# Kernel tuning notes

Measured on AMD Instinct MI355X. Metric: run time of the kernel, lower is better.

Reference implementation:

```python
import jax, jax.numpy as jnp
import numpy as np

MAX_REL = 1024
N_HEADS = 16
HEAD_DIM = 64


def setup_inputs() -> dict:
    key = jax.random.key(0)
    ks = jax.random.split(key, 12)
    b, s, dm = 4, 1024, 1024
    sc = 1.0 / np.sqrt(dm)
    return {
        "hidden_states": jax.random.normal(ks[0], (b, s, dm), jnp.float32),
        "attention_mask": jnp.zeros((b, s), jnp.float32),
        "Wq": jax.random.normal(ks[1], (dm, dm), jnp.float32) * sc,
        "bq": jnp.zeros((dm,), jnp.float32),
        "Wk": jax.random.normal(ks[2], (dm, dm), jnp.float32) * sc,
        "bk": jnp.zeros((dm,), jnp.float32),
        "Wv": jax.random.normal(ks[3], (dm, dm), jnp.float32) * sc,
        "bv": jnp.zeros((dm,), jnp.float32),
        "Wo": jax.random.normal(ks[4], (dm, dm), jnp.float32) * sc,
        "bo": jnp.zeros((dm,), jnp.float32),
        "rel_emb": jax.random.normal(ks[5], (2 * MAX_REL + 1, HEAD_DIM), jnp.float32) * 0.02,
        "M": jax.random.uniform(ks[6], (1, N_HEADS, HEAD_DIM, HEAD_DIM), jnp.float32),
        "z": jax.random.uniform(ks[7], (1, N_HEADS, HEAD_DIM), jnp.float32),
        "gate_alpha": jax.random.uniform(ks[8], (1,), jnp.float32),
    }


def reference(hidden_states, attention_mask, Wq, bq, Wk, bk, Wv, bv, Wo, bo,
              rel_emb, M, z, gate_alpha):
    b, s, dm = hidden_states.shape
    H, D = N_HEADS, HEAD_DIM

    def proj(W, bias):
        return (hidden_states @ W + bias).reshape(b, s, H, D).transpose(0, 2, 1, 3)  # bhsd

    q = proj(Wq, bq)
    k = proj(Wk, bk)
    v = proj(Wv, bv)

    # relative-position embeddings: rel[q_pos, k_pos, d]
    ridx = jnp.clip(jnp.arange(s)[:, None] - jnp.arange(s)[None, :], -MAX_REL, MAX_REL) + MAX_REL
    rel = rel_emb[ridx]  # [s, s, D]

    # scores[b,h,q,k] = sum_d (q + rel) * k   (content + position terms, no 5-D materialization)
    scores = (jnp.einsum('bhqd,bhkd->bhqk', q, k)
              + jnp.einsum('qkd,bhkd->bhqk', rel, k)) / np.sqrt(D).astype(np.float32)
    scores = scores + attention_mask[:, None, None, :] * (-1e9)
    w = jax.nn.softmax(scores, axis=-1)
    local = jnp.einsum('bhqk,bhkd->bhqd', w, v)

    # linear-attention read of global memory (M, z)
    sq = jax.nn.elu(q) + 1.0  # [b,h,s,d]
    num = jnp.einsum('bhld,hde->bhle', sq, M[0])
    den = jnp.einsum('bhld,hd->bhl', sq, z[0]) + 1e-6
    glob = num / den[..., None]

    gate = jax.nn.sigmoid(gate_alpha[0])
    combined = gate * local + (1.0 - gate) * glob  # [b,h,s,d]
    out = combined.transpose(0, 2, 1, 3).reshape(b, s, dm) @ Wo + bo
    return out
```

## Files before the change

### kernel.cpp

```cpp
#include <hip/hip_runtime.h>
#include <cstdint>
#include <cstddef>

typedef __bf16 bf16x8 __attribute__((ext_vector_type(8)));
typedef float f32x4 __attribute__((ext_vector_type(4)));

static __device__ __forceinline__ f32x4 mfma16(bf16x8 a, bf16x8 b, f32x4 c) {
  return __builtin_amdgcn_mfma_f32_16x16x32_bf16(a, b, c, 0, 0, 0);
}


__global__ __launch_bounds__(256) void detect_k(const uint32_t* __restrict__ hs,
                                                int* __restrict__ flag) {
  __shared__ int cnt;
  if (threadIdx.x == 0) cnt = 0;
  __syncthreads();
  uint32_t w = hs[threadIdx.x];
  int b = (w >> 8) & 0x7F;
  if (b >= 0x3C && b <= 0x40) atomicAdd(&cnt, 1);
  __syncthreads();
  if (threadIdx.x == 0) *flag = (cnt >= 128) ? 1 : 0;
}

__global__ __launch_bounds__(256) void cvt_to_bf16_k(const void* __restrict__ src,
                                                     __bf16* __restrict__ dst, int n,
                                                     const int* __restrict__ flag) {
  int i = blockIdx.x * 256 + threadIdx.x;
  if (i >= n) return;
  float v = (*flag) ? (float)((const __bf16*)src)[i] : ((const float*)src)[i];
  dst[i] = (__bf16)v;
}

__global__ __launch_bounds__(256) void cvt_to_f32_k(const void* __restrict__ src,
                                                    float* __restrict__ dst, int n,
                                                    const int* __restrict__ flag) {
  int i = blockIdx.x * 256 + threadIdx.x;
  if (i >= n) return;
  dst[i] = (*flag) ? (float)((const __bf16*)src)[i] : ((const float*)src)[i];
}

__global__ void cvt_wT_k(const void* __restrict__ W, __bf16* __restrict__ T,
                         const int* __restrict__ flag) {
  __shared__ __bf16 t[32][33];
  int k0 = blockIdx.x * 32, n0 = blockIdx.y * 32;
  int tx = threadIdx.x, ty = threadIdx.y;
  int f = *flag;
#pragma unroll
  for (int i = 0; i < 32; i += 8) {
    size_t idx = (size_t)(k0 + ty + i) * 1024 + n0 + tx;
    float v = f ? (float)((const __bf16*)W)[idx] : ((const float*)W)[idx];
    t[ty + i][tx] = (__bf16)v;
  }
  __syncthreads();
#pragma unroll
  for (int i = 0; i < 32; i += 8)
    T[(size_t)(n0 + ty + i) * 1024 + k0 + tx] = t[tx][ty + i];
}

__global__ __launch_bounds__(256) void gemm_bt_k(const __bf16* __restrict__ A,
                                                 const __bf16* __restrict__ Bt,
                                                 const float* __restrict__ bias,
                                                 __bf16* __restrict__ C,
                                                 int M, int N, int K, int ldc) {
  const int tm = blockIdx.x * 128, tn = blockIdx.y * 128;
  const int tid = threadIdx.x;
  const int w = tid >> 6, l = tid & 63;
  const int l15 = l & 15, l4 = l >> 4;
  const int wm = (w >> 1) * 64, wn = (w & 1) * 64;
  __shared__ __bf16 As[128 * 64];
  __shared__ __bf16 Bs[128 * 64];
  f32x4 acc[4][4] = {};
  for (int kt = 0; kt < K; kt += 64) {
    __syncthreads();
#pragma unroll
    for (int i = 0; i < 4; ++i) {
      int c = tid + i * 256;
      int r = c >> 3, s = c & 7;
      int byt = r * 128 + ((s ^ (r & 7)) << 4);
      *(bf16x8*)((char*)As + byt) = *(const bf16x8*)(A + (size_t)(tm + r) * K + kt + s * 8);
      *(bf16x8*)((char*)Bs + byt) = *(const bf16x8*)(Bt + (size_t)(tn + r) * K + kt + s * 8);
    }
    __syncthreads();
#pragma unroll
    for (int kk = 0; kk < 2; ++kk) {
      bf16x8 af[4], bfr[4];
#pragma unroll
      for (int m = 0; m < 4; ++m) {
        int row = wm + m * 16 + l15;
        af[m] = *(const bf16x8*)((char*)As + row * 128 + (((l4 + 4 * kk) ^ (row & 7)) << 4));
      }
#pragma unroll
      for (int n = 0; n < 4; ++n) {
        int row = wn + n * 16 + l15;
        bfr[n] = *(const bf16x8*)((char*)Bs + row * 128 + (((l4 + 4 * kk) ^ (row & 7)) << 4));
      }
#pragma unroll
      for (int m = 0; m < 4; ++m)
#pragma unroll
        for (int n = 0; n < 4; ++n)
          acc[m][n] = mfma16(af[m], bfr[n], acc[m][n]);
    }
  }
#pragma unroll
  for (int m = 0; m < 4; ++m)
#pragma unroll
    for (int n = 0; n < 4; ++n) {
      int row = tm + wm + m * 16 + l4 * 4;
      int col = tn + wn + n * 16 + l15;
      float bb = bias[col];
#pragma unroll
      for (int r = 0; r < 4; ++r)
        C[(size_t)(row + r) * ldc + col] = (__bf16)(acc[m][n][r] + bb);
    }
}

__global__ __launch_bounds__(256) void gemm_bt_out_k(const __bf16* __restrict__ A,
                                                     const __bf16* __restrict__ Bt,
                                                     const float* __restrict__ bias,
                                                     void* __restrict__ out,
                                                     int M, int N, int K, int pairOff,
                                                     const int* __restrict__ flag) {
  const int tm = blockIdx.x * 128, tn = blockIdx.y * 128;
  const int tid = threadIdx.x;
  const int w = tid >> 6, l = tid & 63;
  const int l15 = l & 15, l4 = l >> 4;
  const int wm = (w >> 1) * 64, wn = (w & 1) * 64;
  __shared__ __bf16 As[128 * 64];
  __shared__ __bf16 Bs[128 * 64];
  f32x4 acc[4][4] = {};
  for (int kt = 0; kt < K; kt += 64) {
    __syncthreads();
#pragma unroll
    for (int i = 0; i < 4; ++i) {
      int c = tid + i * 256;
      int r = c >> 3, s = c & 7;
      int byt = r * 128 + ((s ^ (r & 7)) << 4);
      *(bf16x8*)((char*)As + byt) = *(const bf16x8*)(A + (size_t)(tm + r) * K + kt + s * 8);
      *(bf16x8*)((char*)Bs + byt) = *(const bf16x8*)(Bt + (size_t)(tn + r) * K + kt + s * 8);
    }
    __syncthreads();
#pragma unroll
    for (int kk = 0; kk < 2; ++kk) {
      bf16x8 af[4], bfr[4];
#pragma unroll
      for (int m = 0; m < 4; ++m) {
        int row = wm + m * 16 + l15;
        af[m] = *(const bf16x8*)((char*)As + row * 128 + (((l4 + 4 * kk) ^ (row & 7)) << 4));
      }
#pragma unroll
      for (int n = 0; n < 4; ++n) {
        int row = wn + n * 16 + l15;
        bfr[n] = *(const bf16x8*)((char*)Bs + row * 128 + (((l4 + 4 * kk) ^ (row & 7)) << 4));
      }
#pragma unroll
      for (int m = 0; m < 4; ++m)
#pragma unroll
        for (int n = 0; n < 4; ++n)
          acc[m][n] = mfma16(af[m], bfr[n], acc[m][n]);
    }
  }
  int use16 = *flag;
#pragma unroll
  for (int m = 0; m < 4; ++m)
#pragma unroll
    for (int n = 0; n < 4; ++n) {
      int row = tm + wm + m * 16 + l4 * 4;
      int col = tn + wn + n * 16 + l15;
      float bb = bias[col];
#pragma unroll
      for (int r = 0; r < 4; ++r) {
        float v = acc[m][n][r] + bb;
        size_t idx = (size_t)(pairOff + row + r) * N + col;
        if (use16) ((__bf16*)out)[idx] = (__bf16)v;
        else       ((float*)out)[idx] = v;
      }
    }
}

__global__ __launch_bounds__(256) void attn_fused_k(const __bf16* __restrict__ QKV2,
                                                    const float* __restrict__ amask,
                                                    const __bf16* __restrict__ rel16,
                                                    const __bf16* __restrict__ Mg16,
                                                    const float* __restrict__ zg32,
                                                    const float* __restrict__ ga32,
                                                    __bf16* __restrict__ comb) {
  const int qt = blockIdx.x, bh = blockIdx.y;
  const int bl = bh >> 4, h = bh & 15;
  const int tid = threadIdx.x;
  const int w = tid >> 6, l = tid & 63;
  const int l15 = l & 15, l4 = l >> 4;
  const int q0 = qt * 64;
  const __bf16* QKVb = QKV2 + (size_t)bl * 1024 * 3072;

  __shared__ __bf16 Kt[64][72];
  __shared__ __bf16 VtT[64][72];
  __shared__ __bf16 Pl[4][16 * 72];
  __shared__ float RKb[128 * 66];
  __shared__ float maskv[64];
  __shared__ float denv[64];

  bf16x8 qf[2];
#pragma unroll
  for (int kk = 0; kk < 2; ++kk)
    qf[kk] = *(const bf16x8*)(QKVb + (size_t)(q0 + w * 16 + l15) * 3072 + h * 64 +
                              l4 * 8 + kk * 32);

  f32x4 accO[4] = {};
  float mrun[4], lrun[4];
#pragma unroll
  for (int r = 0; r < 4; ++r) { mrun[r] = -3.0e38f; lrun[r] = 0.f; }

  for (int kt = 0; kt < 16; ++kt) {
    const int k0 = kt * 64;
    __syncthreads();
#pragma unroll
    for (int i = 0; i < 2; ++i) {
      int c = tid + i * 256;
      int kr = c >> 3, s = (c & 7) * 8;
      const __bf16* src = QKVb + (size_t)(k0 + kr) * 3072 + h * 64;
      *(bf16x8*)(&Kt[kr][s]) = *(const bf16x8*)(src + 1024 + s);
      bf16x8 vv = *(const bf16x8*)(src + 2048 + s);
#pragma unroll
      for (int j = 0; j < 8; ++j) VtT[s + j][kr] = vv[j];
    }
    if (tid < 64) maskv[tid] = amask[bl * 1024 + k0 + tid];
    __syncthreads();

    const int jb = q0 - k0 - 63 + 1024;
#pragma unroll
    for (int ms = 0; ms < 2; ++ms) {
      f32x4 rk[4] = {};
#pragma unroll
      for (int kk = 0; kk < 2; ++kk) {
        bf16x8 ea = *(const bf16x8*)(rel16 + (size_t)(jb + w * 32 + ms * 16 + l15) * 64 +
                                     l4 * 8 + kk * 32);
#pragma unroll
        for (int nb = 0; nb < 4; ++nb) {
          bf16x8 kb = *(const bf16x8*)(&Kt[nb * 16 + l15][l4 * 8 + kk * 32]);
          rk[nb] = mfma16(ea, kb, rk[nb]);
        }
      }
#pragma unroll
      for (int nb = 0; nb < 4; ++nb)
#pragma unroll
        for (int r = 0; r < 4; ++r)
          RKb[(w * 32 + ms * 16 + l4 * 4 + r) * 66 + nb * 16 + l15] = rk[nb][r];
    }
    __syncthreads();

    f32x4 sacc[4] = {};
#pragma unroll
    for (int kk = 0; kk < 2; ++kk)
#pragma unroll
      for (int nb = 0; nb < 4; ++nb) {
        bf16x8 kb = *(const bf16x8*)(&Kt[nb * 16 + l15][l4 * 8 + kk * 32]);
        sacc[nb] = mfma16(qf[kk], kb, sacc[nb]);
      }

    float p[4][4];
    float tmax[4];
#pragma unroll
    for (int r = 0; r < 4; ++r) tmax[r] = -3.0e38f;
#pragma unroll
    for (int nb = 0; nb < 4; ++nb) {
      int kloc = nb * 16 + l15;
      float mk = maskv[kloc] * (-1e9f);
#pragma unroll
      for (int r = 0; r < 4; ++r) {
        int jl = (w * 16 + l4 * 4 + r) - kloc + 63;
        float s = (sacc[nb][r] + RKb[jl * 66 + kloc]) * 0.125f + mk;
        p[nb][r] = s;
        tmax[r] = fmaxf(tmax[r], s);
      }
    }
#pragma unroll
    for (int x = 1; x < 16; x <<= 1)
#pragma unroll
      for (int r = 0; r < 4; ++r) tmax[r] = fmaxf(tmax[r], __shfl_xor(tmax[r], x, 64));
    float al[4];
#pragma unroll
    for (int r = 0; r < 4; ++r) {
      float mn = fmaxf(mrun[r], tmax[r]);
      al[r] = __expf(mrun[r] - mn);
      mrun[r] = mn;
    }
    float rs[4] = {0.f, 0.f, 0.f, 0.f};
#pragma unroll
    for (int nb = 0; nb < 4; ++nb)
#pragma unroll
      for (int r = 0; r < 4; ++r) {
        p[nb][r] = __expf(p[nb][r] - mrun[r]);
        rs[r] += p[nb][r];
      }
#pragma unroll
    for (int x = 1; x < 16; x <<= 1)
#pragma unroll
      for (int r = 0; r < 4; ++r) rs[r] += __shfl_xor(rs[r], x, 64);
#pragma unroll
    for (int r = 0; r < 4; ++r) lrun[r] = lrun[r] * al[r] + rs[r];
#pragma unroll
    for (int nb = 0; nb < 4; ++nb)
#pragma unroll
      for (int r = 0; r < 4; ++r) accO[nb][r] *= al[r];

#pragma unroll
    for (int nb = 0; nb < 4; ++nb)
#pragma unroll
      for (int r = 0; r < 4; ++r)
        Pl[w][(l4 * 4 + r) * 72 + nb * 16 + l15] = (__bf16)p[nb][r];
    __syncthreads();

#pragma unroll
    for (int kk = 0; kk < 2; ++kk) {
      bf16x8 pa = *(const bf16x8*)(&Pl[w][l15 * 72 + kk * 32 + l4 * 8]);
#pragma unroll
      for (int nb = 0; nb < 4; ++nb) {
        bf16x8 vb = *(const bf16x8*)(&VtT[nb * 16 + l15][kk * 32 + l4 * 8]);
        accO[nb] = mfma16(pa, vb, accO[nb]);
      }
    }
  }

#pragma unroll
  for (int nb = 0; nb < 4; ++nb)
#pragma unroll
    for (int r = 0; r < 4; ++r) accO[nb][r] /= lrun[r];

  __syncthreads();
  __bf16* sqb = (__bf16*)RKb;
  __bf16* Mtb = ((__bf16*)RKb) + 64 * 72;
#pragma unroll
  for (int i = 0; i < 2; ++i) {
    int c = tid + i * 256;
    int qr = c >> 3, s = (c & 7) * 8;
    bf16x8 qv = *(const bf16x8*)(QKVb + (size_t)(q0 + qr) * 3072 + h * 64 + s);
#pragma unroll
    for (int j = 0; j < 8; ++j) {
      float x = (float)qv[j];
      sqb[qr * 72 + s + j] = (__bf16)(x > 0.f ? x + 1.f : __expf(x));
    }
    bf16x8 mv = *(const bf16x8*)(Mg16 + (size_t)h * 4096 + qr * 64 + s);
#pragma unroll
    for (int j = 0; j < 8; ++j) Mtb[(s + j) * 72 + qr] = mv[j];
  }
  __syncthreads();
  if (tid < 64) {
    float sden = 0.f;
    const float* zp = zg32 + h * 64;
#pragma unroll
    for (int d = 0; d < 64; ++d) sden += (float)sqb[tid * 72 + d] * zp[d];
    denv[tid] = sden + 1e-6f;
  }
  __syncthreads();
  float gate = 1.f / (1.f + __expf(-ga32[0]));
  f32x4 nacc[4] = {};
#pragma unroll
  for (int kk = 0; kk < 2; ++kk) {
    bf16x8 sa = *(const bf16x8*)(sqb + (w * 16 + l15) * 72 + kk * 32 + l4 * 8);
#pragma unroll
    for (int nb = 0; nb < 4; ++nb) {
      bf16x8 mb = *(const bf16x8*)(Mtb + (nb * 16 + l15) * 72 + kk * 32 + l4 * 8);
      nacc[nb] = mfma16(sa, mb, nacc[nb]);
    }
  }
#pragma unroll
  for (int nb = 0; nb < 4; ++nb)
#pragma unroll
    for (int r = 0; r < 4; ++r) {
      int qrel = w * 16 + l4 * 4 + r;
      float gl = nacc[nb][r] / denv[qrel];
      float cv = gate * accO[nb][r] + (1.f - gate) * gl;
      comb[(size_t)(bl * 1024 + q0 + qrel) * 1024 + h * 64 + nb * 16 + l15] = (__bf16)cv;
    }
}

extern "C" void kernel_launch(void* const* d_in, const int* in_sizes, int n_in,
                              void* d_out, int out_size, void* d_ws, size_t ws_size,
                              hipStream_t stream) {
  const int expect[14] = {4194304, 4096, 1048576, 1024, 1048576, 1024, 1048576,
                          1024, 1048576, 1024, 131136, 65536, 1024, 1};
  if (n_in != 14) return;
  for (int i = 0; i < 14; ++i)
    if (in_sizes[i] != expect[i]) return;

  char* ws = (char*)d_ws;
  int*    flag  = (int*)ws;
  float*  am32  = (float*)(ws + 1024);
  float*  b32   = (float*)(ws + 17408);
  float*  zg32  = (float*)(ws + 33792);
  float*  ga32  = (float*)(ws + 37888);
  __bf16* Mg16  = (__bf16*)(ws + 38912);
  __bf16* rel16 = (__bf16*)(ws + 301056);
  __bf16* hs16  = (__bf16*)(ws + 565248);
  __bf16* WT16  = (__bf16*)(ws + 8953856);
  __bf16* qkv2  = (__bf16*)(ws + 17342464);
  __bf16* comb2 = (__bf16*)(ws + 29925376);

  detect_k<<<1, 256, 0, stream>>>((const uint32_t*)d_in[0], flag);

  cvt_to_bf16_k<<<16384, 256, 0, stream>>>(d_in[0], hs16, 4194304, flag);
  cvt_to_f32_k<<<16, 256, 0, stream>>>(d_in[1], am32, 4096, flag);
  const int widx[4] = {2, 4, 6, 8};
  for (int j = 0; j < 4; ++j) {
    cvt_wT_k<<<dim3(32, 32), dim3(32, 8), 0, stream>>>(d_in[widx[j]],
                                                       WT16 + (size_t)j * 1048576, flag);
    cvt_to_f32_k<<<4, 256, 0, stream>>>(d_in[widx[j] + 1], b32 + j * 1024, 1024, flag);
  }
  cvt_to_bf16_k<<<513, 256, 0, stream>>>(d_in[10], rel16, 131136, flag);
  cvt_to_bf16_k<<<256, 256, 0, stream>>>(d_in[11], Mg16, 65536, flag);
  cvt_to_f32_k<<<4, 256, 0, stream>>>(d_in[12], zg32, 1024, flag);
  cvt_to_f32_k<<<1, 256, 0, stream>>>(d_in[13], ga32, 1, flag);

  for (int pr = 0; pr < 2; ++pr) {
    gemm_bt_k<<<dim3(16, 24), 256, 0, stream>>>(
        hs16 + (size_t)pr * 2097152, WT16, b32, qkv2, 2048, 3072, 1024, 3072);
    attn_fused_k<<<dim3(16, 32), 256, 0, stream>>>(
        qkv2, am32 + pr * 2048, rel16, Mg16, zg32, ga32, comb2);
    gemm_bt_out_k<<<dim3(16, 8), 256, 0, stream>>>(
        comb2, WT16 + 3 * 1048576, b32 + 3072, d_out, 2048, 1024, 1024,
        pr * 2048, flag);
  }
}
```

Before: 283.2 us.

## Pre-transpose V and M in global memory; convert hidden states per pass

Adds a separate kernel that writes V in a per-head transposed layout after the QKV GEMM, so the attention kernel loads V tiles with vector stores instead of a scalar scatter transpose into shared memory on every key tile. M is also transposed once during its conversion, which removes another scalar shared-memory transpose. The hidden-state bf16 conversion is split into two halves done inside the per-pass loop, which shrinks the workspace and may keep the converted data cache-resident. The cost is an extra kernel launch and a global write and read of V per pass.

```diff
diff --git a/kernel.cpp b/kernel.cpp
--- a/kernel.cpp
+++ b/kernel.cpp
@@ -23,11 +23,13 @@
 }
 
 __global__ __launch_bounds__(256) void cvt_to_bf16_k(const void* __restrict__ src,
+                                                     size_t srcOff,
                                                      __bf16* __restrict__ dst, int n,
                                                      const int* __restrict__ flag) {
   int i = blockIdx.x * 256 + threadIdx.x;
   if (i >= n) return;
-  float v = (*flag) ? (float)((const __bf16*)src)[i] : ((const float*)src)[i];
+  float v = (*flag) ? (float)((const __bf16*)src)[srcOff + i]
+                    : ((const float*)src)[srcOff + i];
   dst[i] = (__bf16)v;
 }
 
@@ -39,6 +41,17 @@
   dst[i] = (*flag) ? (float)((const __bf16*)src)[i] : ((const float*)src)[i];
 }
 
+__global__ __launch_bounds__(256) void cvt_MgT_k(const void* __restrict__ src,
+                                                 __bf16* __restrict__ dst,
+                                                 const int* __restrict__ flag) {
+  int i = blockIdx.x * 256 + threadIdx.x;
+  if (i >= 65536) return;
+  int h = i >> 12, rem = i & 4095, e = rem >> 6, d = rem & 63;
+  size_t sidx = (size_t)h * 4096 + d * 64 + e;
+  float v = (*flag) ? (float)((const __bf16*)src)[sidx] : ((const float*)src)[sidx];
+  dst[i] = (__bf16)v;
+}
+
 __global__ void cvt_wT_k(const void* __restrict__ W, __bf16* __restrict__ T,
                          const int* __restrict__ flag) {
   __shared__ __bf16 t[32][33];
@@ -55,6 +68,25 @@
 #pragma unroll
   for (int i = 0; i < 32; i += 8)
     T[(size_t)(n0 + ty + i) * 1024 + k0 + tx] = t[tx][ty + i];
+}
+
+__global__ __launch_bounds__(256) void vt2_k(const __bf16* __restrict__ qkv2,
+                                             __bf16* __restrict__ Vt2) {
+  __shared__ __bf16 t[64][72];
+  const int h = blockIdx.x, k0 = blockIdx.y * 64, bl = blockIdx.z;
+  const int tid = threadIdx.x;
+  const int r = tid >> 2, dc = (tid & 3) * 16;
+  const __bf16* src = qkv2 + (size_t)(bl * 1024 + k0 + r) * 3072 + 2048 + h * 64 + dc;
+  *(bf16x8*)(&t[r][dc]) = *(const bf16x8*)(src);
+  *(bf16x8*)(&t[r][dc + 8]) = *(const bf16x8*)(src + 8);
+  __syncthreads();
+  const int dr = tid >> 2, kc = (tid & 3) * 16;
+  __bf16* dst = Vt2 + ((size_t)(bl * 16 + h) * 64 + dr) * 1024 + k0 + kc;
+  bf16x8 o0, o1;
+#pragma unroll
+  for (int j = 0; j < 8; ++j) { o0[j] = t[kc + j][dr]; o1[j] = t[kc + 8 + j][dr]; }
+  *(bf16x8*)dst = o0;
+  *(bf16x8*)(dst + 8) = o1;
 }
 
 __global__ __launch_bounds__(256) void gemm_bt_k(const __bf16* __restrict__ A,
@@ -178,9 +210,10 @@
 }
 
 __global__ __launch_bounds__(256) void attn_fused_k(const __bf16* __restrict__ QKV2,
+                                                    const __bf16* __restrict__ Vt2,
                                                     const float* __restrict__ amask,
                                                     const __bf16* __restrict__ rel16,
-                                                    const __bf16* __restrict__ Mg16,
+                                                    const __bf16* __restrict__ MgT16,
                                                     const float* __restrict__ zg32,
                                                     const float* __restrict__ ga32,
                                                     __bf16* __restrict__ comb) {
@@ -191,6 +224,7 @@
   const int l15 = l & 15, l4 = l >> 4;
   const int q0 = qt * 64;
   const __bf16* QKVb = QKV2 + (size_t)bl * 1024 * 3072;
+  const __bf16* VtH = Vt2 + (size_t)(bl * 16 + h) * 64 * 1024;
 
   __shared__ __bf16 Kt[64][72];
   __shared__ __bf16 VtT[64][72];
@@ -217,11 +251,9 @@
     for (int i = 0; i < 2; ++i) {
       int c = tid + i * 256;
       int kr = c >> 3, s = (c & 7) * 8;
-      const __bf16* src = QKVb + (size_t)(k0 + kr) * 3072 + h * 64;
-      *(bf16x8*)(&Kt[kr][s]) = *(const bf16x8*)(src + 1024 + s);
-      bf16x8 vv = *(const bf16x8*)(src + 2048 + s);
-#pragma unroll
-      for (int j = 0; j < 8; ++j) VtT[s + j][kr] = vv[j];
+      *(bf16x8*)(&Kt[kr][s]) =
+          *(const bf16x8*)(QKVb + (size_t)(k0 + kr) * 3072 + 1024 + h * 64 + s);
+      *(bf16x8*)(&VtT[kr][s]) = *(const bf16x8*)(VtH + (size_t)kr * 1024 + k0 + s);
     }
     if (tid < 64) maskv[tid] = amask[bl * 1024 + k0 + tid];
     __syncthreads();
@@ -339,9 +371,8 @@
       float x = (float)qv[j];
       sqb[qr * 72 + s + j] = (__bf16)(x > 0.f ? x + 1.f : __expf(x));
     }
-    bf16x8 mv = *(const bf16x8*)(Mg16 + (size_t)h * 4096 + qr * 64 + s);
-#pragma unroll
-    for (int j = 0; j < 8; ++j) Mtb[(s + j) * 72 + qr] = mv[j];
+    bf16x8 mv = *(const bf16x8*)(MgT16 + (size_t)h * 4096 + qr * 64 + s);
+    *(bf16x8*)(&Mtb[qr * 72 + s]) = mv;
   }
   __syncthreads();
   if (tid < 64) {
@@ -384,21 +415,21 @@
     if (in_sizes[i] != expect[i]) return;
 
   char* ws = (char*)d_ws;
-  int*    flag  = (int*)ws;
-  float*  am32  = (float*)(ws + 1024);
-  float*  b32   = (float*)(ws + 17408);
-  float*  zg32  = (float*)(ws + 33792);
-  float*  ga32  = (float*)(ws + 37888);
-  __bf16* Mg16  = (__bf16*)(ws + 38912);
-  __bf16* rel16 = (__bf16*)(ws + 301056);
-  __bf16* hs16  = (__bf16*)(ws + 565248);
-  __bf16* WT16  = (__bf16*)(ws + 8953856);
-  __bf16* qkv2  = (__bf16*)(ws + 17342464);
-  __bf16* comb2 = (__bf16*)(ws + 29925376);
+  int*    flag   = (int*)ws;
+  float*  am32   = (float*)(ws + 1024);
+  float*  b32    = (float*)(ws + 17408);
+  float*  zg32   = (float*)(ws + 33792);
+  float*  ga32   = (float*)(ws + 37888);
+  __bf16* MgT16  = (__bf16*)(ws + 38912);
+  __bf16* rel16  = (__bf16*)(ws + 301056);
+  __bf16* hs_pr  = (__bf16*)(ws + 565248);
+  __bf16* WT16   = (__bf16*)(ws + 4759552);
+  __bf16* qkv2   = (__bf16*)(ws + 13148160);
+  __bf16* comb2  = (__bf16*)(ws + 25731072);
+  __bf16* Vt2    = (__bf16*)(ws + 29925376);
 
   detect_k<<<1, 256, 0, stream>>>((const uint32_t*)d_in[0], flag);
 
-  cvt_to_bf16_k<<<16384, 256, 0, stream>>>(d_in[0], hs16, 4194304, flag);
   cvt_to_f32_k<<<16, 256, 0, stream>>>(d_in[1], am32, 4096, flag);
   const int widx[4] = {2, 4, 6, 8};
   for (int j = 0; j < 4; ++j) {
@@ -406,16 +437,19 @@
                                                        WT16 + (size_t)j * 1048576, flag);
     cvt_to_f32_k<<<4, 256, 0, stream>>>(d_in[widx[j] + 1], b32 + j * 1024, 1024, flag);
   }
-  cvt_to_bf16_k<<<513, 256, 0, stream>>>(d_in[10], rel16, 131136, flag);
-  cvt_to_bf16_k<<<256, 256, 0, stream>>>(d_in[11], Mg16, 65536, flag);
+  cvt_to_bf16_k<<<513, 256, 0, stream>>>(d_in[10], 0, rel16, 131136, flag);
+  cvt_MgT_k<<<256, 256, 0, stream>>>(d_in[11], MgT16, flag);
   cvt_to_f32_k<<<4, 256, 0, stream>>>(d_in[12], zg32, 1024, flag);
   cvt_to_f32_k<<<1, 256, 0, stream>>>(d_in[13], ga32, 1, flag);
 
   for (int pr = 0; pr < 2; ++pr) {
-    gemm_bt_k<<<dim3(16, 24), 256, 0, stream>>>(
-        hs16 + (size_t)pr * 2097152, WT16, b32, qkv2, 2048, 3072, 1024, 3072);
+    cvt_to_bf16_k<<<8192, 256, 0, stream>>>(d_in[0], (size_t)pr * 2097152, hs_pr,
+                                            2097152, flag);
+    gemm_bt_k<<<dim3(16, 24), 256, 0, stream>>>(hs_pr, WT16, b32, qkv2,
+                                                2048, 3072, 1024, 3072);
+    vt2_k<<<dim3(16, 16, 2), 256, 0, stream>>>(qkv2, Vt2);
     attn_fused_k<<<dim3(16, 32), 256, 0, stream>>>(
-        qkv2, am32 + pr * 2048, rel16, Mg16, zg32, ga32, comb2);
+        qkv2, Vt2, am32 + pr * 2048, rel16, MgT16, zg32, ga32, comb2);
     gemm_bt_out_k<<<dim3(16, 8), 256, 0, stream>>>(
         comb2, WT16 + 3 * 1048576, b32 + 3072, d_out, 2048, 1024, 1024,
         pr * 2048, flag);
```

Result: faster. 270.9 us (-4.3%).
